# Optimization experiments

Hardware: AMD Instinct MI355X
Metric: run time of the kernel (lower is better)

The kernel has to match this reference:

```python
import jax, jax.numpy as jnp
import numpy as np

N_NODES = 50000
N_EDGES = 600000
IN_DIM = 128
HID = 128
OUT_DIM = 2


def _init_linear(key, out_dim, in_dim):
    scale = 1.0 / np.sqrt(in_dim)
    return jax.random.uniform(key, (out_dim, in_dim), jnp.float32, -scale, scale)


def setup_inputs() -> dict:
    key = jax.random.key(0)
    ks = jax.random.split(key, 12)
    x = jax.random.normal(ks[0], (N_NODES, IN_DIM), jnp.float32)
    edge_index = jax.random.randint(ks[1], (2, N_EDGES), 0, N_NODES, jnp.int64)
    dims = [(HID, IN_DIM), (HID, HID), (OUT_DIM, HID)]
    inp = {"x": x, "edge_index": edge_index}
    for i, (o, d) in enumerate(dims):
        inp[f"Wl{i}"] = _init_linear(ks[2 + 3 * i], o, d)      # lin_l: applied to aggregated neighbors
        inp[f"Wr{i}"] = _init_linear(ks[3 + 3 * i], o, d)      # lin_r: applied to root (self) features
        inp[f"b{i}"] = jnp.zeros((o,), jnp.float32)            # bias of lin_l
    return inp


def _sage_conv(x, src, dst, Wl, Wr, b):
    # mean-aggregate source features onto target nodes, then linear transform
    msgs = x[src]                                              # [E, d] gather
    agg = jax.ops.segment_sum(msgs, dst, num_segments=N_NODES)
    cnt = jax.ops.segment_sum(jnp.ones((src.shape[0], 1), x.dtype), dst,
                              num_segments=N_NODES)
    agg = agg / jnp.maximum(cnt, 1.0)                          # mean over in-edges
    return agg @ Wl.T + b + x @ Wr.T


def reference(x, edge_index, Wl0, Wr0, b0, Wl1, Wr1, b1, Wl2, Wr2, b2):
    src, dst = edge_index[0], edge_index[1]
    # eval mode: dropout is identity
    h = jax.nn.relu(_sage_conv(x, src, dst, Wl0, Wr0, b0))
    h = jax.nn.relu(_sage_conv(h, src, dst, Wl1, Wr1, b1))
    return _sage_conv(h, src, dst, Wl2, Wr2, b2)
```

## Files before the change

kernel.cpp:

```cpp
#include <hip/hip_runtime.h>
#include <hip/hip_bf16.h>

#define N_NODES 50000
#define N_EDGES 600000
#define DIM 128
#define CAP 64

typedef short bf16x8 __attribute__((ext_vector_type(8)));
typedef float f32x4 __attribute__((ext_vector_type(4)));

__device__ __forceinline__ ushort f2b(float f) {
    __hip_bfloat16 h = __float2bfloat16(f);
    return *reinterpret_cast<ushort*>(&h);
}
__device__ __forceinline__ float b2f_lo(unsigned u) { return __uint_as_float(u << 16); }
__device__ __forceinline__ float b2f_hi(unsigned u) { return __uint_as_float(u & 0xffff0000u); }

static constexpr size_t alignup(size_t x) { return (x + 255) & ~size_t(255); }
static constexpr size_t OFF_FLAG = 0;
static constexpr size_t OFF_CNT  = 256;
static constexpr size_t OFF_COL  = alignup(OFF_CNT + sizeof(unsigned) * N_NODES);
static constexpr size_t OFF_XBF  = alignup(OFF_COL + sizeof(int) * (size_t)N_NODES * CAP);
static constexpr size_t OFF_AGG  = alignup(OFF_XBF + sizeof(ushort) * N_NODES * DIM);
static constexpr size_t OFF_H1   = alignup(OFF_AGG + sizeof(ushort) * N_NODES * DIM);
static constexpr size_t OFF_H2   = alignup(OFF_H1 + sizeof(ushort) * N_NODES * DIM);
static constexpr size_t OFF_WL0  = alignup(OFF_H2 + sizeof(ushort) * N_NODES * DIM);
static constexpr size_t OFF_WR0  = alignup(OFF_WL0 + sizeof(ushort) * DIM * DIM);
static constexpr size_t OFF_WL1  = alignup(OFF_WR0 + sizeof(ushort) * DIM * DIM);
static constexpr size_t OFF_WR1  = alignup(OFF_WL1 + sizeof(ushort) * DIM * DIM);

__global__ __launch_bounds__(256) void prep_k(const int* __restrict__ ei,
                                              const float* __restrict__ x,
                                              const float* __restrict__ wa, const float* __restrict__ wb,
                                              const float* __restrict__ wc, const float* __restrict__ wd,
                                              unsigned* __restrict__ flag,
                                              unsigned* __restrict__ cnt,
                                              ushort* __restrict__ xbf,
                                              ushort* __restrict__ oa, ushort* __restrict__ ob,
                                              ushort* __restrict__ oc, ushort* __restrict__ od) {
    const int bid = blockIdx.x, t = threadIdx.x;
    if (bid < 6250) {
        const int i = bid * 256 + t;
        float4 v = reinterpret_cast<const float4*>(x)[i];
        ushort4 o;
        o.x = f2b(v.x); o.y = f2b(v.y); o.z = f2b(v.z); o.w = f2b(v.w);
        reinterpret_cast<ushort4*>(xbf)[i] = o;
        if (i < N_NODES) cnt[i] = 0u;
        if (bid == 0) {
            __shared__ unsigned any;
            if (t == 0) any = 0u;
            __syncthreads();
            unsigned hv = 0;
#pragma unroll
            for (int j = 0; j < 4; ++j) hv |= (unsigned)ei[2 * (t * 4 + j) + 1];
            if (hv) atomicOr(&any, 1u);
            __syncthreads();
            if (t == 0) *flag = any;
        }
    } else {
        const int wb_i = bid - 6250;
        const int w = wb_i >> 4;
        const float* src = (w == 0) ? wa : (w == 1) ? wb : (w == 2) ? wc : wd;
        ushort* dst      = (w == 0) ? oa : (w == 1) ? ob : (w == 2) ? oc : od;
        const int i = (wb_i & 15) * 256 + t;
        float4 v = reinterpret_cast<const float4*>(src)[i];
        ushort4 o;
        o.x = f2b(v.x); o.y = f2b(v.y); o.z = f2b(v.z); o.w = f2b(v.w);
        reinterpret_cast<ushort4*>(dst)[i] = o;
    }
}

__global__ void fillcsr_k(const int* __restrict__ ei, const unsigned* __restrict__ flag,
                          unsigned* __restrict__ cnt, int* __restrict__ col) {
    int e0 = (blockIdx.x * 256 + threadIdx.x) * 4;
    if (e0 >= N_EDGES) return;
    int s[4], d[4];
    if (*flag) {
        uint4 sv = *reinterpret_cast<const uint4*>(&ei[e0]);
        uint4 dv = *reinterpret_cast<const uint4*>(&ei[N_EDGES + e0]);
        s[0] = sv.x; s[1] = sv.y; s[2] = sv.z; s[3] = sv.w;
        d[0] = dv.x; d[1] = dv.y; d[2] = dv.z; d[3] = dv.w;
    } else {
        uint4 sa = *reinterpret_cast<const uint4*>(&ei[2 * e0]);
        uint4 sb = *reinterpret_cast<const uint4*>(&ei[2 * e0 + 4]);
        uint4 da = *reinterpret_cast<const uint4*>(&ei[2 * (N_EDGES + e0)]);
        uint4 db = *reinterpret_cast<const uint4*>(&ei[2 * (N_EDGES + e0) + 4]);
        s[0] = sa.x; s[1] = sa.z; s[2] = sb.x; s[3] = sb.z;
        d[0] = da.x; d[1] = da.z; d[2] = db.x; d[3] = db.z;
    }
#pragma unroll
    for (int i = 0; i < 4; ++i) {
        unsigned pos = atomicAdd(&cnt[d[i]], 1u);
        if (pos < CAP) col[(size_t)d[i] * CAP + pos] = s[i];
    }
}

__global__ __launch_bounds__(256) void agg_k(const ushort* __restrict__ h,
                                             const unsigned* __restrict__ cnt,
                                             const int* __restrict__ col,
                                             ushort* __restrict__ aggm) {
    const int g = threadIdx.x >> 4, lane = threadIdx.x & 15;
    const int node = blockIdx.x * 16 + g;
    if (node >= N_NODES) return;
    unsigned deg = cnt[node];
    if (deg > CAP) deg = CAP;
    const int* cp = &col[(size_t)node * CAP];
    float acc[8];
#pragma unroll
    for (int i = 0; i < 8; ++i) acc[i] = 0.f;
    const int co = lane * 8;
    unsigned e = 0;
    for (; e + 4 <= deg; e += 4) {
        const int s0 = cp[e], s1 = cp[e + 1], s2 = cp[e + 2], s3 = cp[e + 3];
        const uint4 v0 = *reinterpret_cast<const uint4*>(&h[(size_t)s0 * DIM + co]);
        const uint4 v1 = *reinterpret_cast<const uint4*>(&h[(size_t)s1 * DIM + co]);
        const uint4 v2 = *reinterpret_cast<const uint4*>(&h[(size_t)s2 * DIM + co]);
        const uint4 v3 = *reinterpret_cast<const uint4*>(&h[(size_t)s3 * DIM + co]);
        acc[0] += b2f_lo(v0.x) + b2f_lo(v1.x) + b2f_lo(v2.x) + b2f_lo(v3.x);
        acc[1] += b2f_hi(v0.x) + b2f_hi(v1.x) + b2f_hi(v2.x) + b2f_hi(v3.x);
        acc[2] += b2f_lo(v0.y) + b2f_lo(v1.y) + b2f_lo(v2.y) + b2f_lo(v3.y);
        acc[3] += b2f_hi(v0.y) + b2f_hi(v1.y) + b2f_hi(v2.y) + b2f_hi(v3.y);
        acc[4] += b2f_lo(v0.z) + b2f_lo(v1.z) + b2f_lo(v2.z) + b2f_lo(v3.z);
        acc[5] += b2f_hi(v0.z) + b2f_hi(v1.z) + b2f_hi(v2.z) + b2f_hi(v3.z);
        acc[6] += b2f_lo(v0.w) + b2f_lo(v1.w) + b2f_lo(v2.w) + b2f_lo(v3.w);
        acc[7] += b2f_hi(v0.w) + b2f_hi(v1.w) + b2f_hi(v2.w) + b2f_hi(v3.w);
    }
    for (; e < deg; ++e) {
        const int s = cp[e];
        const uint4 v = *reinterpret_cast<const uint4*>(&h[(size_t)s * DIM + co]);
        acc[0] += b2f_lo(v.x); acc[1] += b2f_hi(v.x);
        acc[2] += b2f_lo(v.y); acc[3] += b2f_hi(v.y);
        acc[4] += b2f_lo(v.z); acc[5] += b2f_hi(v.z);
        acc[6] += b2f_lo(v.w); acc[7] += b2f_hi(v.w);
    }
    const float inv = 1.0f / fmaxf((float)deg, 1.0f);
    uint4 o;
    o.x = (unsigned)f2b(acc[0] * inv) | ((unsigned)f2b(acc[1] * inv) << 16);
    o.y = (unsigned)f2b(acc[2] * inv) | ((unsigned)f2b(acc[3] * inv) << 16);
    o.z = (unsigned)f2b(acc[4] * inv) | ((unsigned)f2b(acc[5] * inv) << 16);
    o.w = (unsigned)f2b(acc[6] * inv) | ((unsigned)f2b(acc[7] * inv) << 16);
    *reinterpret_cast<uint4*>(&aggm[(size_t)node * DIM + co]) = o;
}

template <bool RELU>
__global__ __launch_bounds__(256) void xform_mfma_k(const ushort* __restrict__ A0,
                                                    const ushort* __restrict__ A1,
                                                    const ushort* __restrict__ Wl,
                                                    const ushort* __restrict__ Wr,
                                                    const float*  __restrict__ bias,
                                                    ushort* __restrict__ hout) {
    __shared__ ushort Ws[128 * 136];
    const int t    = threadIdx.x;
    const int wave = t >> 6;
    const int l    = t & 63;
    const int l16  = l & 15;
    const int lk   = (l >> 4) * 8;
    const int node = blockIdx.x * 64 + wave * 16 + l16;
    const bool valid = node < N_NODES;

    const int wrow = t >> 1;
    const int wc0  = (t & 1) * 64;

    f32x4 acc[8];
#pragma unroll
    for (int i = 0; i < 8; ++i) acc[i] = (f32x4){0.f, 0.f, 0.f, 0.f};

    const bf16x8 zfrag = (bf16x8){0, 0, 0, 0, 0, 0, 0, 0};

#pragma unroll
    for (int p = 0; p < 2; ++p) {
        const ushort* Asrc = p ? A1 : A0;
        const ushort* Wsrc = p ? Wr : Wl;

        bf16x8 bf[4];
#pragma unroll
        for (int ks = 0; ks < 4; ++ks)
            bf[ks] = valid
                ? *reinterpret_cast<const bf16x8*>(&Asrc[(size_t)node * DIM + ks * 32 + lk])
                : zfrag;

        __syncthreads();
        {
            const uint4* src = reinterpret_cast<const uint4*>(&Wsrc[(size_t)wrow * DIM + wc0]);
            uint4* dst = reinterpret_cast<uint4*>(&Ws[wrow * 136 + wc0]);
#pragma unroll
            for (int i = 0; i < 8; ++i) dst[i] = src[i];
        }
        __syncthreads();

#pragma unroll
        for (int ks = 0; ks < 4; ++ks) {
            const int kb = ks * 32;
#pragma unroll
            for (int ot = 0; ot < 8; ++ot) {
                const bf16x8 afrag = *reinterpret_cast<const bf16x8*>(
                    &Ws[(ot * 16 + l16) * 136 + kb + lk]);
                acc[ot] = __builtin_amdgcn_mfma_f32_16x16x32_bf16(afrag, bf[ks], acc[ot], 0, 0, 0);
            }
        }
    }

    if (!valid) return;
    const int orow = (l >> 4) * 4;
#pragma unroll
    for (int ot = 0; ot < 8; ++ot) {
        const float4 b4 = *reinterpret_cast<const float4*>(&bias[ot * 16 + orow]);
        float r0 = acc[ot][0] + b4.x;
        float r1 = acc[ot][1] + b4.y;
        float r2 = acc[ot][2] + b4.z;
        float r3 = acc[ot][3] + b4.w;
        if (RELU) {
            r0 = fmaxf(r0, 0.f); r1 = fmaxf(r1, 0.f);
            r2 = fmaxf(r2, 0.f); r3 = fmaxf(r3, 0.f);
        }
        ushort4 s;
        s.x = f2b(r0); s.y = f2b(r1); s.z = f2b(r2); s.w = f2b(r3);
        *reinterpret_cast<ushort4*>(&hout[(size_t)node * DIM + ot * 16 + orow]) = s;
    }
}

__global__ __launch_bounds__(256) void out2_fused_k(const ushort* __restrict__ h,
                                                    const unsigned* __restrict__ cnt,
                                                    const int* __restrict__ col,
                                                    const float* __restrict__ Wl,
                                                    const float* __restrict__ Wr,
                                                    const float* __restrict__ bias,
                                                    float* __restrict__ out) {
    __shared__ float wl[256], wr[256];
    const int t = threadIdx.x;
    wl[t] = Wl[t];
    wr[t] = Wr[t];
    __syncthreads();
    const int g = t >> 4, lane = t & 15;
    const int node = blockIdx.x * 16 + g;
    if (node >= N_NODES) return;
    unsigned deg = cnt[node];
    if (deg > CAP) deg = CAP;
    const int* cp = &col[(size_t)node * CAP];
    const int co = lane * 8;
    float acc[8];
#pragma unroll
    for (int i = 0; i < 8; ++i) acc[i] = 0.f;
    unsigned e = 0;
    for (; e + 4 <= deg; e += 4) {
        const int s0 = cp[e], s1 = cp[e + 1], s2 = cp[e + 2], s3 = cp[e + 3];
        const uint4 v0 = *reinterpret_cast<const uint4*>(&h[(size_t)s0 * DIM + co]);
        const uint4 v1 = *reinterpret_cast<const uint4*>(&h[(size_t)s1 * DIM + co]);
        const uint4 v2 = *reinterpret_cast<const uint4*>(&h[(size_t)s2 * DIM + co]);
        const uint4 v3 = *reinterpret_cast<const uint4*>(&h[(size_t)s3 * DIM + co]);
        acc[0] += b2f_lo(v0.x) + b2f_lo(v1.x) + b2f_lo(v2.x) + b2f_lo(v3.x);
        acc[1] += b2f_hi(v0.x) + b2f_hi(v1.x) + b2f_hi(v2.x) + b2f_hi(v3.x);
        acc[2] += b2f_lo(v0.y) + b2f_lo(v1.y) + b2f_lo(v2.y) + b2f_lo(v3.y);
        acc[3] += b2f_hi(v0.y) + b2f_hi(v1.y) + b2f_hi(v2.y) + b2f_hi(v3.y);
        acc[4] += b2f_lo(v0.z) + b2f_lo(v1.z) + b2f_lo(v2.z) + b2f_lo(v3.z);
        acc[5] += b2f_hi(v0.z) + b2f_hi(v1.z) + b2f_hi(v2.z) + b2f_hi(v3.z);
        acc[6] += b2f_lo(v0.w) + b2f_lo(v1.w) + b2f_lo(v2.w) + b2f_lo(v3.w);
        acc[7] += b2f_hi(v0.w) + b2f_hi(v1.w) + b2f_hi(v2.w) + b2f_hi(v3.w);
    }
    for (; e < deg; ++e) {
        const int s = cp[e];
        const uint4 v = *reinterpret_cast<const uint4*>(&h[(size_t)s * DIM + co]);
        acc[0] += b2f_lo(v.x); acc[1] += b2f_hi(v.x);
        acc[2] += b2f_lo(v.y); acc[3] += b2f_hi(v.y);
        acc[4] += b2f_lo(v.z); acc[5] += b2f_hi(v.z);
        acc[6] += b2f_lo(v.w); acc[7] += b2f_hi(v.w);
    }
    const float inv = 1.0f / fmaxf((float)deg, 1.0f);
    const uint4 rv = *reinterpret_cast<const uint4*>(&h[(size_t)node * DIM + co]);
    float root[8];
    root[0] = b2f_lo(rv.x); root[1] = b2f_hi(rv.x);
    root[2] = b2f_lo(rv.y); root[3] = b2f_hi(rv.y);
    root[4] = b2f_lo(rv.z); root[5] = b2f_hi(rv.z);
    root[6] = b2f_lo(rv.w); root[7] = b2f_hi(rv.w);
    float p0 = 0.f, p1 = 0.f;
#pragma unroll
    for (int j = 0; j < 8; ++j) {
        const float av = acc[j] * inv;
        p0 += av * wl[co + j] + root[j] * wr[co + j];
        p1 += av * wl[128 + co + j] + root[j] * wr[128 + co + j];
    }
#pragma unroll
    for (int m = 1; m < 16; m <<= 1) {
        p0 += __shfl_xor(p0, m);
        p1 += __shfl_xor(p1, m);
    }
    if (lane == 0) {
        out[(size_t)node * 2 + 0] = p0 + bias[0];
        out[(size_t)node * 2 + 1] = p1 + bias[1];
    }
}

extern "C" void kernel_launch(void* const* d_in, const int* in_sizes, int n_in,
                              void* d_out, int out_size, void* d_ws, size_t ws_size,
                              hipStream_t stream) {
    const float* x   = (const float*)d_in[0];
    const int*   ei  = (const int*)d_in[1];
    const float* Wl0 = (const float*)d_in[2];
    const float* Wr0 = (const float*)d_in[3];
    const float* b0  = (const float*)d_in[4];
    const float* Wl1 = (const float*)d_in[5];
    const float* Wr1 = (const float*)d_in[6];
    const float* b1  = (const float*)d_in[7];
    const float* Wl2 = (const float*)d_in[8];
    const float* Wr2 = (const float*)d_in[9];
    const float* b2  = (const float*)d_in[10];

    char* ws = (char*)d_ws;
    unsigned* flag = (unsigned*)(ws + OFF_FLAG);
    unsigned* cnt  = (unsigned*)(ws + OFF_CNT);
    int*      col  = (int*)(ws + OFF_COL);
    ushort*   xbf  = (ushort*)(ws + OFF_XBF);
    ushort*   aggm = (ushort*)(ws + OFF_AGG);
    ushort*   h1   = (ushort*)(ws + OFF_H1);
    ushort*   h2   = (ushort*)(ws + OFF_H2);
    ushort*   wl0b = (ushort*)(ws + OFF_WL0);
    ushort*   wr0b = (ushort*)(ws + OFF_WR0);
    ushort*   wl1b = (ushort*)(ws + OFF_WL1);
    ushort*   wr1b = (ushort*)(ws + OFF_WR1);
    float*    out  = (float*)d_out;

    prep_k<<<6250 + 64, 256, 0, stream>>>(ei, x, Wl0, Wr0, Wl1, Wr1,
                                          flag, cnt, xbf, wl0b, wr0b, wl1b, wr1b);
    fillcsr_k<<<(N_EDGES / 4 + 255) / 256, 256, 0, stream>>>(ei, flag, cnt, col);

    agg_k<<<(N_NODES + 15) / 16, 256, 0, stream>>>(xbf, cnt, col, aggm);
    xform_mfma_k<true><<<(N_NODES + 63) / 64, 256, 0, stream>>>(aggm, xbf, wl0b, wr0b, b0, h1);
    agg_k<<<(N_NODES + 15) / 16, 256, 0, stream>>>(h1, cnt, col, aggm);
    xform_mfma_k<true><<<(N_NODES + 63) / 64, 256, 0, stream>>>(aggm, h1, wl1b, wr1b, b1, h2);
    out2_fused_k<<<(N_NODES + 15) / 16, 256, 0, stream>>>(h2, cnt, col, Wl2, Wr2, b2, out);
}
```

Measured before the change: 152.8 us.

## Project layer-2 features to output dim before aggregation and fuse into layer-1 transform

Because mean aggregation is linear, the final layer now applies Wl2 and Wr2 to h2 inside the second MFMA transform epilogue, producing per-node 2-wide projections. The last aggregation then gathers only 2 floats per edge instead of 128 bf16 values. The h2 write and re-read are removed as well. In exchange, the transform epilogue does extra LDS reads and cross-lane shuffle reductions, and the summation order changes slightly.

After: 133.7 us. 1.14x faster.

```diff
diff --git a/kernel.cpp b/kernel.cpp
--- a/kernel.cpp
+++ b/kernel.cpp
@@ -23,8 +23,9 @@
 static constexpr size_t OFF_XBF  = alignup(OFF_COL + sizeof(int) * (size_t)N_NODES * CAP);
 static constexpr size_t OFF_AGG  = alignup(OFF_XBF + sizeof(ushort) * N_NODES * DIM);
 static constexpr size_t OFF_H1   = alignup(OFF_AGG + sizeof(ushort) * N_NODES * DIM);
-static constexpr size_t OFF_H2   = alignup(OFF_H1 + sizeof(ushort) * N_NODES * DIM);
-static constexpr size_t OFF_WL0  = alignup(OFF_H2 + sizeof(ushort) * N_NODES * DIM);
+static constexpr size_t OFF_Z    = alignup(OFF_H1 + sizeof(ushort) * N_NODES * DIM);
+static constexpr size_t OFF_RT   = alignup(OFF_Z + sizeof(float) * 2 * N_NODES);
+static constexpr size_t OFF_WL0  = alignup(OFF_RT + sizeof(float) * 2 * N_NODES);
 static constexpr size_t OFF_WR0  = alignup(OFF_WL0 + sizeof(ushort) * DIM * DIM);
 static constexpr size_t OFF_WL1  = alignup(OFF_WR0 + sizeof(ushort) * DIM * DIM);
 static constexpr size_t OFF_WR1  = alignup(OFF_WL1 + sizeof(ushort) * DIM * DIM);
@@ -142,7 +143,6 @@
     *reinterpret_cast<uint4*>(&aggm[(size_t)node * DIM + co]) = o;
 }
 
-template <bool RELU>
 __global__ __launch_bounds__(256) void xform_mfma_k(const ushort* __restrict__ A0,
                                                     const ushort* __restrict__ A1,
                                                     const ushort* __restrict__ Wl,
@@ -205,88 +205,135 @@
 #pragma unroll
     for (int ot = 0; ot < 8; ++ot) {
         const float4 b4 = *reinterpret_cast<const float4*>(&bias[ot * 16 + orow]);
-        float r0 = acc[ot][0] + b4.x;
-        float r1 = acc[ot][1] + b4.y;
-        float r2 = acc[ot][2] + b4.z;
-        float r3 = acc[ot][3] + b4.w;
-        if (RELU) {
-            r0 = fmaxf(r0, 0.f); r1 = fmaxf(r1, 0.f);
-            r2 = fmaxf(r2, 0.f); r3 = fmaxf(r3, 0.f);
-        }
+        float r0 = fmaxf(acc[ot][0] + b4.x, 0.f);
+        float r1 = fmaxf(acc[ot][1] + b4.y, 0.f);
+        float r2 = fmaxf(acc[ot][2] + b4.z, 0.f);
+        float r3 = fmaxf(acc[ot][3] + b4.w, 0.f);
         ushort4 s;
         s.x = f2b(r0); s.y = f2b(r1); s.z = f2b(r2); s.w = f2b(r3);
         *reinterpret_cast<ushort4*>(&hout[(size_t)node * DIM + ot * 16 + orow]) = s;
     }
 }
 
-__global__ __launch_bounds__(256) void out2_fused_k(const ushort* __restrict__ h,
-                                                    const unsigned* __restrict__ cnt,
-                                                    const int* __restrict__ col,
-                                                    const float* __restrict__ Wl,
-                                                    const float* __restrict__ Wr,
-                                                    const float* __restrict__ bias,
-                                                    float* __restrict__ out) {
-    __shared__ float wl[256], wr[256];
-    const int t = threadIdx.x;
-    wl[t] = Wl[t];
-    wr[t] = Wr[t];
-    __syncthreads();
-    const int g = t >> 4, lane = t & 15;
-    const int node = blockIdx.x * 16 + g;
+__global__ __launch_bounds__(256) void xform_final_k(const ushort* __restrict__ A0,
+                                                     const ushort* __restrict__ A1,
+                                                     const ushort* __restrict__ Wl,
+                                                     const ushort* __restrict__ Wr,
+                                                     const float*  __restrict__ bias,
+                                                     const float*  __restrict__ Wl2,
+                                                     const float*  __restrict__ Wr2,
+                                                     const float*  __restrict__ b2,
+                                                     float* __restrict__ z,
+                                                     float* __restrict__ rt) {
+    __shared__ ushort Ws[128 * 136];
+    __shared__ float wl2s[256], wr2s[256];
+    const int t    = threadIdx.x;
+    const int wave = t >> 6;
+    const int l    = t & 63;
+    const int l16  = l & 15;
+    const int lk   = (l >> 4) * 8;
+    const int node = blockIdx.x * 64 + wave * 16 + l16;
+    const bool valid = node < N_NODES;
+
+    const int wrow = t >> 1;
+    const int wc0  = (t & 1) * 64;
+
+    wl2s[t] = Wl2[t];
+    wr2s[t] = Wr2[t];
+
+    f32x4 acc[8];
+#pragma unroll
+    for (int i = 0; i < 8; ++i) acc[i] = (f32x4){0.f, 0.f, 0.f, 0.f};
+
+    const bf16x8 zfrag = (bf16x8){0, 0, 0, 0, 0, 0, 0, 0};
+
+#pragma unroll
+    for (int p = 0; p < 2; ++p) {
+        const ushort* Asrc = p ? A1 : A0;
+        const ushort* Wsrc = p ? Wr : Wl;
+
+        bf16x8 bf[4];
+#pragma unroll
+        for (int ks = 0; ks < 4; ++ks)
+            bf[ks] = valid
+                ? *reinterpret_cast<const bf16x8*>(&Asrc[(size_t)node * DIM + ks * 32 + lk])
+                : zfrag;
+
+        __syncthreads();
+        {
+            const uint4* src = reinterpret_cast<const uint4*>(&Wsrc[(size_t)wrow * DIM + wc0]);
+            uint4* dst = reinterpret_cast<uint4*>(&Ws[wrow * 136 + wc0]);
+#pragma unroll
+            for (int i = 0; i < 8; ++i) dst[i] = src[i];
+        }
+        __syncthreads();
+
+#pragma unroll
+        for (int ks = 0; ks < 4; ++ks) {
+            const int kb = ks * 32;
+#pragma unroll
+            for (int ot = 0; ot < 8; ++ot) {
+                const bf16x8 afrag = *reinterpret_cast<const bf16x8*>(
+                    &Ws[(ot * 16 + l16) * 136 + kb + lk]);
+                acc[ot] = __builtin_amdgcn_mfma_f32_16x16x32_bf16(afrag, bf[ks], acc[ot], 0, 0, 0);
+            }
+        }
+    }
+
+    const int orow = (l >> 4) * 4;
+    float z0 = 0.f, z1 = 0.f, r0s = 0.f, r1s = 0.f;
+#pragma unroll
+    for (int ot = 0; ot < 8; ++ot) {
+        const int o = ot * 16 + orow;
+        const float4 b4 = *reinterpret_cast<const float4*>(&bias[o]);
+        const float h0 = fmaxf(acc[ot][0] + b4.x, 0.f);
+        const float h1v = fmaxf(acc[ot][1] + b4.y, 0.f);
+        const float h2v = fmaxf(acc[ot][2] + b4.z, 0.f);
+        const float h3 = fmaxf(acc[ot][3] + b4.w, 0.f);
+        z0  += h0 * wl2s[o] + h1v * wl2s[o + 1] + h2v * wl2s[o + 2] + h3 * wl2s[o + 3];
+        z1  += h0 * wl2s[128 + o] + h1v * wl2s[128 + o + 1] + h2v * wl2s[128 + o + 2] + h3 * wl2s[128 + o + 3];
+        r0s += h0 * wr2s[o] + h1v * wr2s[o + 1] + h2v * wr2s[o + 2] + h3 * wr2s[o + 3];
+        r1s += h0 * wr2s[128 + o] + h1v * wr2s[128 + o + 1] + h2v * wr2s[128 + o + 2] + h3 * wr2s[128 + o + 3];
+    }
+    z0  += __shfl_xor(z0, 16);  z0  += __shfl_xor(z0, 32);
+    z1  += __shfl_xor(z1, 16);  z1  += __shfl_xor(z1, 32);
+    r0s += __shfl_xor(r0s, 16); r0s += __shfl_xor(r0s, 32);
+    r1s += __shfl_xor(r1s, 16); r1s += __shfl_xor(r1s, 32);
+    if ((l >> 4) == 0 && valid) {
+        float2 zv = {z0, z1};
+        float2 rv = {r0s + b2[0], r1s + b2[1]};
+        *reinterpret_cast<float2*>(&z[(size_t)node * 2])  = zv;
+        *reinterpret_cast<float2*>(&rt[(size_t)node * 2]) = rv;
+    }
+}
+
+__global__ __launch_bounds__(256) void outgather_k(const float* __restrict__ z,
+                                                   const float* __restrict__ rt,
+                                                   const unsigned* __restrict__ cnt,
+                                                   const int* __restrict__ col,
+                                                   float* __restrict__ out) {
+    const int g = threadIdx.x >> 3, lane = threadIdx.x & 7;
+    const int node = blockIdx.x * 32 + g;
     if (node >= N_NODES) return;
     unsigned deg = cnt[node];
     if (deg > CAP) deg = CAP;
     const int* cp = &col[(size_t)node * CAP];
-    const int co = lane * 8;
-    float acc[8];
-#pragma unroll
-    for (int i = 0; i < 8; ++i) acc[i] = 0.f;
-    unsigned e = 0;
-    for (; e + 4 <= deg; e += 4) {
-        const int s0 = cp[e], s1 = cp[e + 1], s2 = cp[e + 2], s3 = cp[e + 3];
-        const uint4 v0 = *reinterpret_cast<const uint4*>(&h[(size_t)s0 * DIM + co]);
-        const uint4 v1 = *reinterpret_cast<const uint4*>(&h[(size_t)s1 * DIM + co]);
-        const uint4 v2 = *reinterpret_cast<const uint4*>(&h[(size_t)s2 * DIM + co]);
-        const uint4 v3 = *reinterpret_cast<const uint4*>(&h[(size_t)s3 * DIM + co]);
-        acc[0] += b2f_lo(v0.x) + b2f_lo(v1.x) + b2f_lo(v2.x) + b2f_lo(v3.x);
-        acc[1] += b2f_hi(v0.x) + b2f_hi(v1.x) + b2f_hi(v2.x) + b2f_hi(v3.x);
-        acc[2] += b2f_lo(v0.y) + b2f_lo(v1.y) + b2f_lo(v2.y) + b2f_lo(v3.y);
-        acc[3] += b2f_hi(v0.y) + b2f_hi(v1.y) + b2f_hi(v2.y) + b2f_hi(v3.y);
-        acc[4] += b2f_lo(v0.z) + b2f_lo(v1.z) + b2f_lo(v2.z) + b2f_lo(v3.z);
-        acc[5] += b2f_hi(v0.z) + b2f_hi(v1.z) + b2f_hi(v2.z) + b2f_hi(v3.z);
-        acc[6] += b2f_lo(v0.w) + b2f_lo(v1.w) + b2f_lo(v2.w) + b2f_lo(v3.w);
-        acc[7] += b2f_hi(v0.w) + b2f_hi(v1.w) + b2f_hi(v2.w) + b2f_hi(v3.w);
-    }
-    for (; e < deg; ++e) {
+    float s0 = 0.f, s1 = 0.f;
+    for (unsigned e = lane; e < deg; e += 8) {
         const int s = cp[e];
-        const uint4 v = *reinterpret_cast<const uint4*>(&h[(size_t)s * DIM + co]);
-        acc[0] += b2f_lo(v.x); acc[1] += b2f_hi(v.x);
-        acc[2] += b2f_lo(v.y); acc[3] += b2f_hi(v.y);
-        acc[4] += b2f_lo(v.z); acc[5] += b2f_hi(v.z);
-        acc[6] += b2f_lo(v.w); acc[7] += b2f_hi(v.w);
-    }
-    const float inv = 1.0f / fmaxf((float)deg, 1.0f);
-    const uint4 rv = *reinterpret_cast<const uint4*>(&h[(size_t)node * DIM + co]);
-    float root[8];
-    root[0] = b2f_lo(rv.x); root[1] = b2f_hi(rv.x);
-    root[2] = b2f_lo(rv.y); root[3] = b2f_hi(rv.y);
-    root[4] = b2f_lo(rv.z); root[5] = b2f_hi(rv.z);
-    root[6] = b2f_lo(rv.w); root[7] = b2f_hi(rv.w);
-    float p0 = 0.f, p1 = 0.f;
-#pragma unroll
-    for (int j = 0; j < 8; ++j) {
-        const float av = acc[j] * inv;
-        p0 += av * wl[co + j] + root[j] * wr[co + j];
-        p1 += av * wl[128 + co + j] + root[j] * wr[128 + co + j];
-    }
-#pragma unroll
-    for (int m = 1; m < 16; m <<= 1) {
-        p0 += __shfl_xor(p0, m);
-        p1 += __shfl_xor(p1, m);
+        const float2 v = *reinterpret_cast<const float2*>(&z[(size_t)s * 2]);
+        s0 += v.x; s1 += v.y;
+    }
+#pragma unroll
+    for (int m = 1; m < 8; m <<= 1) {
+        s0 += __shfl_xor(s0, m);
+        s1 += __shfl_xor(s1, m);
     }
     if (lane == 0) {
-        out[(size_t)node * 2 + 0] = p0 + bias[0];
-        out[(size_t)node * 2 + 1] = p1 + bias[1];
+        const float inv = 1.0f / fmaxf((float)deg, 1.0f);
+        const float2 rv = *reinterpret_cast<const float2*>(&rt[(size_t)node * 2]);
+        float2 o = {s0 * inv + rv.x, s1 * inv + rv.y};
+        *reinterpret_cast<float2*>(&out[(size_t)node * 2]) = o;
     }
 }
 
@@ -312,7 +359,8 @@
     ushort*   xbf  = (ushort*)(ws + OFF_XBF);
     ushort*   aggm = (ushort*)(ws + OFF_AGG);
     ushort*   h1   = (ushort*)(ws + OFF_H1);
-    ushort*   h2   = (ushort*)(ws + OFF_H2);
+    float*    zbuf = (float*)(ws + OFF_Z);
+    float*    rtb  = (float*)(ws + OFF_RT);
     ushort*   wl0b = (ushort*)(ws + OFF_WL0);
     ushort*   wr0b = (ushort*)(ws + OFF_WR0);
     ushort*   wl1b = (ushort*)(ws + OFF_WL1);
@@ -324,8 +372,9 @@
     fillcsr_k<<<(N_EDGES / 4 + 255) / 256, 256, 0, stream>>>(ei, flag, cnt, col);
 
     agg_k<<<(N_NODES + 15) / 16, 256, 0, stream>>>(xbf, cnt, col, aggm);
-    xform_mfma_k<true><<<(N_NODES + 63) / 64, 256, 0, stream>>>(aggm, xbf, wl0b, wr0b, b0, h1);
+    xform_mfma_k<<<(N_NODES + 63) / 64, 256, 0, stream>>>(aggm, xbf, wl0b, wr0b, b0, h1);
     agg_k<<<(N_NODES + 15) / 16, 256, 0, stream>>>(h1, cnt, col, aggm);
-    xform_mfma_k<true><<<(N_NODES + 63) / 64, 256, 0, stream>>>(aggm, h1, wl1b, wr1b, b1, h2);
-    out2_fused_k<<<(N_NODES + 15) / 16, 256, 0, stream>>>(h2, cnt, col, Wl2, Wr2, b2, out);
-}
+    xform_final_k<<<(N_NODES + 63) / 64, 256, 0, stream>>>(aggm, h1, wl1b, wr1b, b1,
+                                                           Wl2, Wr2, b2, zbuf, rtb);
+    outgather_k<<<(N_NODES + 31) / 32, 256, 0, stream>>>(zbuf, rtb, cnt, col, out);
+}
```
